# Kernel optimization log

Hardware: AMD Instinct MI355X
Metric: run time of the kernel (lower is better)

## Reference

```python
import jax, jax.numpy as jnp
import numpy as np

T1 = 8      # list[index-1]
T2 = 8      # list[index]
L = 8
GAMA = 1.0
EPS = -8e-05

@jax.custom_vjp
def zif(u):
    return (u >= EPS).astype(u.dtype)

def _zif_fwd(u):
    return zif(u), u

def _zif_bwd(u, g):
    tmp = (1.0 / GAMA) * (1.0 / GAMA) * jnp.clip(GAMA - jnp.abs(u), a_min=0.0)
    return (g * tmp,)

zif.defvjp(_zif_fwd, _zif_bwd)


def setup_inputs() -> dict:
    key = jax.random.key(0)
    k1, k2 = jax.random.split(key)
    x = jax.random.uniform(k1, (T1 * 32, 128, 32, 32), dtype=jnp.float32)
    thresh = jnp.ones((1,), dtype=jnp.float32)  # nn.Parameter([1.0])
    return {"x": x, "thresh": thresh}


def _if_forward(x, thresh):
    # thre = thresh.data / L  (detached in the original)
    thre = jax.lax.stop_gradient(thresh) / L          # [1]
    # expand: [T1*B, C, H, W] -> [T1, B, C, H, W]
    B = x.shape[0] // T1
    x_seq = x.reshape((T1, B) + x.shape[1:])
    frame_shape = x_seq.shape[1:]

    mem0 = jnp.broadcast_to(0.5 * thre, frame_shape).astype(x.dtype)
    sc0 = jnp.zeros(frame_shape, dtype=x.dtype)

    # Phase 1: integrate-and-fire over the T1 input frames
    def step1(carry, xt):
        mem, sc = carry
        mem = mem + xt
        spike = zif(mem - thre) * thre
        mem = mem - spike
        return (mem, sc + spike), None
    (mem, sc), _ = jax.lax.scan(step1, (mem0, sc0), x_seq)

    # Phase 2: T3-1 relaxation steps with reverse spikes (hard, no surrogate)
    T3 = max(T1, T2)
    def step2(carry, _):
        mem, sc = carry
        spike = zif(mem - thre) * thre
        rev = (-mem > 0).astype(mem.dtype) * thre
        mem = mem - spike + rev
        return (mem, sc + spike - rev), None
    (mem, sc), _ = jax.lax.scan(step2, (mem, sc), None, length=T3 - 1)

    # Phase 3: re-emit spike_count as T2 output spikes
    def step3(mem, _):
        spike = zif(mem - thre) * thre
        return mem - spike, spike
    _, spike_pot = jax.lax.scan(step3, sc, None, length=T2)  # [T2, B, C, H, W]

    # merge: flatten(0, 1)
    return spike_pot.reshape((T2 * B,) + frame_shape[1:])


def reference(x, thresh):
    return _if_forward(x, thresh)
```

## Files before the change

kernel.cpp:

```cpp
#include <hip/hip_runtime.h>


#define T1 8
#define T2 8
#define L_DIV 8.0f
#define EPS_C (-8e-05f)
#define G 2

typedef float fvec4 __attribute__((ext_vector_type(4)));

__global__ __launch_bounds__(256) void if_fwd_fused(
    const fvec4* __restrict__ x,
    const float* __restrict__ thresh,
    fvec4* __restrict__ out,
    int n4)
{
    const int base = blockIdx.x * (256 * G) + threadIdx.x;
    const float thre = thresh[0] / L_DIV;

    fvec4 xv[G][T1];
    #pragma unroll
    for (int t = 0; t < T1; ++t)
        #pragma unroll
        for (int g = 0; g < G; ++g)
            xv[g][t] = __builtin_nontemporal_load(&x[(size_t)t * n4 + base + g * 256]);

    float m[G][4], sc[G][4];
    #pragma unroll
    for (int g = 0; g < G; ++g)
        #pragma unroll
        for (int k = 0; k < 4; ++k) { m[g][k] = 0.5f * thre; sc[g][k] = 0.0f; }

    #pragma unroll
    for (int t = 0; t < T1; ++t)
        #pragma unroll
        for (int g = 0; g < G; ++g)
            #pragma unroll
            for (int k = 0; k < 4; ++k) {
                m[g][k] += xv[g][t][k];
                const float spike = (m[g][k] - thre >= EPS_C) ? thre : 0.0f;
                m[g][k] -= spike;
                sc[g][k] += spike;
            }

    #pragma unroll
    for (int t = 0; t < T1 - 1; ++t)
        #pragma unroll
        for (int g = 0; g < G; ++g)
            #pragma unroll
            for (int k = 0; k < 4; ++k) {
                const float spike = (m[g][k] - thre >= EPS_C) ? thre : 0.0f;
                const float rev   = (-m[g][k] > 0.0f) ? thre : 0.0f;
                m[g][k] = m[g][k] - spike + rev;
                sc[g][k] += spike - rev;
            }

    #pragma unroll
    for (int t = 0; t < T2; ++t) {
        const float cut = (float)(t + 1) * thre;
        #pragma unroll
        for (int g = 0; g < G; ++g) {
            fvec4 o;
            #pragma unroll
            for (int k = 0; k < 4; ++k)
                o[k] = (sc[g][k] - cut >= EPS_C) ? thre : 0.0f;
            out[(size_t)t * n4 + base + g * 256] = o;
        }
    }
}

extern "C" void kernel_launch(void* const* d_in, const int* in_sizes, int n_in,
                              void* d_out, int out_size, void* d_ws, size_t ws_size,
                              hipStream_t stream) {
    const fvec4* x      = (const fvec4*)d_in[0];
    const float* thresh = (const float*)d_in[1];
    fvec4*       out    = (fvec4*)d_out;

    const int N  = in_sizes[0] / T1;
    const int n4 = N / 4;

    const int block = 256;
    const int grid  = n4 / (block * G);
    if_fwd_fused<<<grid, block, 0, stream>>>(x, thresh, out, n4);
}
```

Before: 225.3 us.

## Split IF kernel into integer spike-count pass and separate emit pass

Splits the fused kernel into two launches. The first integrates inputs and keeps an integer spike count, writing one byte per element to workspace. The second reads those counts and writes the output spikes with nontemporal stores. The intent is to separate the read-heavy and write-heavy phases and simplify the emit logic. In exchange it adds a second launch and an extra workspace round trip, and it falls back to the fused kernel when no workspace is provided.

```diff
diff --git a/kernel.cpp b/kernel.cpp
--- a/kernel.cpp
+++ b/kernel.cpp
@@ -8,6 +8,84 @@
 #define G 2
 
 typedef float fvec4 __attribute__((ext_vector_type(4)));
+typedef char  cvec4 __attribute__((ext_vector_type(4)));
+
+__global__ __launch_bounds__(256) void if_count(
+    const fvec4* __restrict__ x,
+    const float* __restrict__ thresh,
+    cvec4* __restrict__ cnt,
+    int n4)
+{
+    const int base = blockIdx.x * (256 * G) + threadIdx.x;
+    const float thre = thresh[0] / L_DIV;
+
+    fvec4 xv[G][T1];
+    #pragma unroll
+    for (int t = 0; t < T1; ++t)
+        #pragma unroll
+        for (int g = 0; g < G; ++g)
+            xv[g][t] = __builtin_nontemporal_load(&x[(size_t)t * n4 + base + g * 256]);
+
+    float m[G][4];
+    int   k[G][4];
+    #pragma unroll
+    for (int g = 0; g < G; ++g)
+        #pragma unroll
+        for (int j = 0; j < 4; ++j) { m[g][j] = 0.5f * thre; k[g][j] = 0; }
+
+    #pragma unroll
+    for (int t = 0; t < T1; ++t)
+        #pragma unroll
+        for (int g = 0; g < G; ++g)
+            #pragma unroll
+            for (int j = 0; j < 4; ++j) {
+                m[g][j] += xv[g][t][j];
+                if (m[g][j] - thre >= EPS_C) { m[g][j] -= thre; k[g][j]++; }
+            }
+
+    #pragma unroll
+    for (int t = 0; t < T1 - 1; ++t)
+        #pragma unroll
+        for (int g = 0; g < G; ++g)
+            #pragma unroll
+            for (int j = 0; j < 4; ++j) {
+                const bool spike = (m[g][j] - thre >= EPS_C);
+                const bool rev   = (-m[g][j] > 0.0f);
+                m[g][j] += (rev ? thre : 0.0f) - (spike ? thre : 0.0f);
+                k[g][j] += (spike ? 1 : 0) - (rev ? 1 : 0);
+            }
+
+    #pragma unroll
+    for (int g = 0; g < G; ++g) {
+        cvec4 c;
+        #pragma unroll
+        for (int j = 0; j < 4; ++j) c[j] = (char)k[g][j];
+        cnt[base + g * 256] = c;
+    }
+}
+
+__global__ __launch_bounds__(256) void if_emit(
+    const cvec4* __restrict__ cnt,
+    const float* __restrict__ thresh,
+    fvec4* __restrict__ out,
+    int n4)
+{
+    const int base = blockIdx.x * (256 * G) + threadIdx.x;
+    const float thre = thresh[0] / L_DIV;
+
+    #pragma unroll
+    for (int g = 0; g < G; ++g) {
+        const cvec4 c = cnt[base + g * 256];
+        #pragma unroll
+        for (int t = 0; t < T2; ++t) {
+            fvec4 o;
+            #pragma unroll
+            for (int j = 0; j < 4; ++j)
+                o[j] = ((int)c[j] > t) ? thre : 0.0f;
+            __builtin_nontemporal_store(o, &out[(size_t)t * n4 + base + g * 256]);
+        }
+    }
+}
 
 __global__ __launch_bounds__(256) void if_fwd_fused(
     const fvec4* __restrict__ x,
@@ -29,18 +107,18 @@
     #pragma unroll
     for (int g = 0; g < G; ++g)
         #pragma unroll
-        for (int k = 0; k < 4; ++k) { m[g][k] = 0.5f * thre; sc[g][k] = 0.0f; }
+        for (int j = 0; j < 4; ++j) { m[g][j] = 0.5f * thre; sc[g][j] = 0.0f; }
 
     #pragma unroll
     for (int t = 0; t < T1; ++t)
         #pragma unroll
         for (int g = 0; g < G; ++g)
             #pragma unroll
-            for (int k = 0; k < 4; ++k) {
-                m[g][k] += xv[g][t][k];
-                const float spike = (m[g][k] - thre >= EPS_C) ? thre : 0.0f;
-                m[g][k] -= spike;
-                sc[g][k] += spike;
+            for (int j = 0; j < 4; ++j) {
+                m[g][j] += xv[g][t][j];
+                const float spike = (m[g][j] - thre >= EPS_C) ? thre : 0.0f;
+                m[g][j] -= spike;
+                sc[g][j] += spike;
             }
 
     #pragma unroll
@@ -48,11 +126,11 @@
         #pragma unroll
         for (int g = 0; g < G; ++g)
             #pragma unroll
-            for (int k = 0; k < 4; ++k) {
-                const float spike = (m[g][k] - thre >= EPS_C) ? thre : 0.0f;
-                const float rev   = (-m[g][k] > 0.0f) ? thre : 0.0f;
-                m[g][k] = m[g][k] - spike + rev;
-                sc[g][k] += spike - rev;
+            for (int j = 0; j < 4; ++j) {
+                const float spike = (m[g][j] - thre >= EPS_C) ? thre : 0.0f;
+                const float rev   = (-m[g][j] > 0.0f) ? thre : 0.0f;
+                m[g][j] = m[g][j] - spike + rev;
+                sc[g][j] += spike - rev;
             }
 
     #pragma unroll
@@ -62,8 +140,8 @@
         for (int g = 0; g < G; ++g) {
             fvec4 o;
             #pragma unroll
-            for (int k = 0; k < 4; ++k)
-                o[k] = (sc[g][k] - cut >= EPS_C) ? thre : 0.0f;
+            for (int j = 0; j < 4; ++j)
+                o[j] = (sc[g][j] - cut >= EPS_C) ? thre : 0.0f;
             out[(size_t)t * n4 + base + g * 256] = o;
         }
     }
@@ -81,5 +159,12 @@
 
     const int block = 256;
     const int grid  = n4 / (block * G);
-    if_fwd_fused<<<grid, block, 0, stream>>>(x, thresh, out, n4);
+
+    if (d_ws != nullptr && ws_size >= (size_t)n4 * 4) {
+        cvec4* cnt = (cvec4*)d_ws;
+        if_count<<<grid, block, 0, stream>>>(x, thresh, cnt, n4);
+        if_emit<<<grid, block, 0, stream>>>(cnt, thresh, out, n4);
+    } else {
+        if_fwd_fused<<<grid, block, 0, stream>>>(x, thresh, out, n4);
+    }
 }
```

Result: no change. 228.6 us (+1.4%).
